# Kernel tuning notes

Hardware: AMD Instinct MI355X
Metric: run time of the kernel (lower is better)

The kernel has to match this reference:

```python
import jax, jax.numpy as jnp
import numpy as np

WEIGHT = 0.1
EPS = 1e-8


def setup_inputs() -> dict:
    key = jax.random.key(0)
    # [B, 3, D, H, W] deformation field
    deformation_field = jax.random.normal(key, (2, 3, 192, 192, 192), dtype=jnp.float32)
    return {"deformation_field": deformation_field}


def reference(deformation_field):
    f = deformation_field
    # jnp.gradient matches torch.gradient defaults: 2nd-order central interior,
    # 1st-order one-sided differences at the edges, unit spacing.
    grad_x = jnp.gradient(f, axis=2)
    grad_y = jnp.gradient(f, axis=3)
    grad_z = jnp.gradient(f, axis=4)

    divergence = grad_x[:, 0:1] + grad_y[:, 1:2] + grad_z[:, 2:3]
    divergence_loss = jnp.mean(divergence ** 2)

    curl_x = grad_z[:, 1:2] - grad_y[:, 2:3]
    curl_y = grad_x[:, 2:3] - grad_z[:, 0:1]
    curl_z = grad_y[:, 0:1] - grad_x[:, 1:2]
    curl_magnitude = jnp.sqrt(curl_x ** 2 + curl_y ** 2 + curl_z ** 2 + EPS)
    curl_loss = jnp.mean(curl_magnitude)

    return WEIGHT * (divergence_loss + curl_loss)
```

## Files before the change

### kernel.cpp

```cpp
#include <hip/hip_runtime.h>


#define DEP 192
#define HGT 192
#define WID 192
#define NB  2

constexpr int SD = HGT * WID;
constexpr int SC = DEP * SD;
constexpr int SB = 3 * SC;
constexpr int W4 = WID / 4;
constexpr int DSEG = 12;
constexpr int NSEG = DEP / DSEG;
constexpr int NG   = NB * NSEG * HGT * W4;
constexpr int NBLK = NG / 256;
constexpr float SCALE = (float)(0.1 / (double)((long long)NB * DEP * HGT * WID));
constexpr float EPS_C = 1e-8f;

struct V4 { float v[4]; };
__device__ __forceinline__ V4 ld4(const float* p) {
    const float4 t = *(const float4*)p;
    V4 r; r.v[0] = t.x; r.v[1] = t.y; r.v[2] = t.z; r.v[3] = t.w; return r;
}

__global__ __launch_bounds__(256, 4) void gcl_kernel(const float* __restrict__ f,
                                                     float* __restrict__ ws) {
    const int g = blockIdx.x * 256 + threadIdx.x;

    int w4 = g % W4;
    int t  = g / W4;
    int h  = t % HGT;
    t /= HGT;
    int ds = t % NSEG;
    int b  = t / NSEG;
    const int w  = w4 * 4;
    const int d0 = ds * DSEG;

    const int   hmi = (h > 0) ? h - 1 : 0;
    const int   hpi = (h < HGT - 1) ? h + 1 : HGT - 1;
    const float sy  = (h == 0 || h == HGT - 1) ? 1.0f : 0.5f;
    const int   dhm = (hmi - h) * WID;
    const int   dhp = (hpi - h) * WID;
    const int   loff = (w > 0) ? -1 : 0;
    const int   roff = (w4 < W4 - 1) ? 4 : 3;
    const float s0w = (w == 0) ? 1.0f : 0.5f;
    const float s3w = (w4 == W4 - 1) ? 1.0f : 0.5f;

    const float* base = f + b * SB + h * WID + w;

    V4 prev[3], cur[3], nxt[3];
    const int pm = (d0 > 0) ? d0 - 1 : 0;
#pragma unroll
    for (int c = 0; c < 3; ++c) {
        const float* pc = base + c * SC;
        prev[c] = ld4(pc + pm * SD);
        cur[c]  = ld4(pc + d0 * SD);
        nxt[c]  = ld4(pc + (d0 + 1) * SD);
    }

    float local = 0.f;

#pragma unroll
    for (int s = 0; s < DSEG; ++s) {
        const int d = d0 + s;

        V4 hm[3], hp[3], nn[3];
        float lv[3], rv[3];
#pragma unroll
        for (int c = 0; c < 3; ++c) {
            const float* pd = base + c * SC + d * SD;
            hm[c] = ld4(pd + dhm);
            hp[c] = ld4(pd + dhp);
            lv[c] = pd[loff];
            rv[c] = pd[roff];
        }
        if (s < DSEG - 1) {
            const int d2 = (d + 2 < DEP) ? d + 2 : DEP - 1;
#pragma unroll
            for (int c = 0; c < 3; ++c)
                nn[c] = ld4(base + c * SC + d2 * SD);
        }

        const float sx = (d == 0 || d == DEP - 1) ? 1.0f : 0.5f;

        float dv[4], cx[4], cy[4], cz[4];
#pragma unroll
        for (int j = 0; j < 4; ++j) {
            dv[j] =  sx * (nxt[0].v[j] - prev[0].v[j]);
            cz[j] = -sx * (nxt[1].v[j] - prev[1].v[j]);
            cy[j] =  sx * (nxt[2].v[j] - prev[2].v[j]);
        }
        {
            float gz0[4], gz1[4], gz2[4];
            gz0[0] = s0w * (cur[0].v[1] - lv[0]);
            gz0[1] = 0.5f * (cur[0].v[2] - cur[0].v[0]);
            gz0[2] = 0.5f * (cur[0].v[3] - cur[0].v[1]);
            gz0[3] = s3w * (rv[0] - cur[0].v[2]);
            gz1[0] = s0w * (cur[1].v[1] - lv[1]);
            gz1[1] = 0.5f * (cur[1].v[2] - cur[1].v[0]);
            gz1[2] = 0.5f * (cur[1].v[3] - cur[1].v[1]);
            gz1[3] = s3w * (rv[1] - cur[1].v[2]);
            gz2[0] = s0w * (cur[2].v[1] - lv[2]);
            gz2[1] = 0.5f * (cur[2].v[2] - cur[2].v[0]);
            gz2[2] = 0.5f * (cur[2].v[3] - cur[2].v[1]);
            gz2[3] = s3w * (rv[2] - cur[2].v[2]);
#pragma unroll
            for (int j = 0; j < 4; ++j) {
                cy[j] -= gz0[j];
                cx[j]  = gz1[j];
                dv[j] += gz2[j];
            }
        }
#pragma unroll
        for (int j = 0; j < 4; ++j) {
            cz[j] += sy * (hp[0].v[j] - hm[0].v[j]);
            dv[j] += sy * (hp[1].v[j] - hm[1].v[j]);
            cx[j] -= sy * (hp[2].v[j] - hm[2].v[j]);
        }
#pragma unroll
        for (int j = 0; j < 4; ++j)
            local += dv[j] * dv[j] +
                     __builtin_amdgcn_sqrtf(cx[j] * cx[j] + cy[j] * cy[j] +
                                            cz[j] * cz[j] + EPS_C);

        if (s < DSEG - 1) {
#pragma unroll
            for (int c = 0; c < 3; ++c) {
                prev[c] = cur[c]; cur[c] = nxt[c]; nxt[c] = nn[c];
            }
        }
    }

#pragma unroll
    for (int off = 32; off > 0; off >>= 1)
        local += __shfl_down(local, off, 64);

    __shared__ float wsum[4];
    const int lane = threadIdx.x & 63;
    const int wv   = threadIdx.x >> 6;
    if (lane == 0) wsum[wv] = local;
    __syncthreads();
    if (threadIdx.x == 0)
        ws[blockIdx.x] = wsum[0] + wsum[1] + wsum[2] + wsum[3];
}

__global__ __launch_bounds__(256) void gcl_reduce(const float* __restrict__ ws,
                                                  float* __restrict__ out) {
    float s = 0.f;
    for (int i = threadIdx.x; i < NBLK; i += 256) s += ws[i];
#pragma unroll
    for (int off = 32; off > 0; off >>= 1)
        s += __shfl_down(s, off, 64);
    __shared__ float wsum[4];
    const int lane = threadIdx.x & 63;
    const int wv   = threadIdx.x >> 6;
    if (lane == 0) wsum[wv] = s;
    __syncthreads();
    if (threadIdx.x == 0)
        out[0] = (wsum[0] + wsum[1] + wsum[2] + wsum[3]) * SCALE;
}

extern "C" void kernel_launch(void* const* d_in, const int* in_sizes, int n_in,
                              void* d_out, int out_size, void* d_ws, size_t ws_size,
                              hipStream_t stream) {
    const float* f = (const float*)d_in[0];
    float* out = (float*)d_out;
    float* ws  = (float*)d_ws;
    gcl_kernel<<<dim3(NBLK), dim3(256), 0, stream>>>(f, ws);
    gcl_reduce<<<dim3(1), dim3(256), 0, stream>>>(ws, out);
}
```

Baseline: 246.5 us.

## Stage 2D tiles in double-buffered LDS for in-plane stencil neighbors

Each block now owns a 16x64 H-W tile and walks 12 depth slices. Each slice is written to double-buffered shared memory along with halo rows and columns. H and W neighbor reads come from LDS instead of redundant global loads. This removes the repeated global and cache traffic for hm/hp/lv/rv, at the cost of one __syncthreads per slice, more LDS use, and divergent halo loads.

New measurement: 577.8 us. +134.4%, slower.

```diff
diff --git a/kernel.cpp b/kernel.cpp
--- a/kernel.cpp
+++ b/kernel.cpp
@@ -9,11 +9,15 @@
 constexpr int SD = HGT * WID;
 constexpr int SC = DEP * SD;
 constexpr int SB = 3 * SC;
-constexpr int W4 = WID / 4;
+constexpr int TH  = 16;
+constexpr int TW4 = 16;
+constexpr int TW  = TW4 * 4;
 constexpr int DSEG = 12;
-constexpr int NSEG = DEP / DSEG;
-constexpr int NG   = NB * NSEG * HGT * W4;
-constexpr int NBLK = NG / 256;
+constexpr int NDS = DEP / DSEG;
+constexpr int NHB = HGT / TH;
+constexpr int NWB = WID / TW;
+constexpr int NBLK = NB * NDS * NHB * NWB;
+constexpr int ROWF = TW + 4;
 constexpr float SCALE = (float)(0.1 / (double)((long long)NB * DEP * HGT * WID));
 constexpr float EPS_C = 1e-8f;
 
@@ -22,100 +26,139 @@
     const float4 t = *(const float4*)p;
     V4 r; r.v[0] = t.x; r.v[1] = t.y; r.v[2] = t.z; r.v[3] = t.w; return r;
 }
+__device__ __forceinline__ void st4(float* p, const V4& a) {
+    *(float4*)p = make_float4(a.v[0], a.v[1], a.v[2], a.v[3]);
+}
 
 __global__ __launch_bounds__(256, 4) void gcl_kernel(const float* __restrict__ f,
                                                      float* __restrict__ ws) {
-    const int g = blockIdx.x * 256 + threadIdx.x;
-
-    int w4 = g % W4;
-    int t  = g / W4;
-    int h  = t % HGT;
-    t /= HGT;
-    int ds = t % NSEG;
-    int b  = t / NSEG;
-    const int w  = w4 * 4;
-    const int d0 = ds * DSEG;
-
-    const int   hmi = (h > 0) ? h - 1 : 0;
-    const int   hpi = (h < HGT - 1) ? h + 1 : HGT - 1;
+    __shared__ float buf[2][3][TH + 2][ROWF];
+    __shared__ float wcol[2][3][TH][2];
+
+    const int tid = threadIdx.x;
+    const int tx = tid & 15;
+    const int ty = tid >> 4;
+
+    int bid = blockIdx.x;
+    const int wb = bid % NWB; bid /= NWB;
+    const int hb = bid % NHB; bid /= NHB;
+    const int dsg = bid % NDS;
+    const int b = bid / NDS;
+
+    const int h0 = hb * TH, w0 = wb * TW, d0 = dsg * DSEG;
+    const int h = h0 + ty;
+    const int w = w0 + tx * 4;
+
     const float sy  = (h == 0 || h == HGT - 1) ? 1.0f : 0.5f;
-    const int   dhm = (hmi - h) * WID;
-    const int   dhp = (hpi - h) * WID;
-    const int   loff = (w > 0) ? -1 : 0;
-    const int   roff = (w4 < W4 - 1) ? 4 : 3;
     const float s0w = (w == 0) ? 1.0f : 0.5f;
-    const float s3w = (w4 == W4 - 1) ? 1.0f : 0.5f;
-
-    const float* base = f + b * SB + h * WID + w;
+    const float s3w = (w + 3 == WID - 1) ? 1.0f : 0.5f;
+
+    const float* fb = f + b * SB;
+    const float* basec = fb + h * WID + w;
+
+    const int  hch  = tid >> 5;
+    const bool hTop = ((tid >> 4) & 1) == 0;
+    const int  htx  = tid & 15;
+    const int  hrow = hTop ? (h0 > 0 ? h0 - 1 : 0)
+                           : (h0 + TH < HGT ? h0 + TH : HGT - 1);
+    const int  hldsrow = hTop ? 0 : TH + 1;
+    const int  cq   = tid - 96;
+    const int  cch  = cq >> 5;
+    const bool cLft = ((cq >> 4) & 1) == 0;
+    const int  crow = cq & 15;
+    const int  ccol = cLft ? (w0 > 0 ? w0 - 1 : 0)
+                           : (w0 + TW < WID ? w0 + TW : WID - 1);
 
     V4 prev[3], cur[3], nxt[3];
     const int pm = (d0 > 0) ? d0 - 1 : 0;
 #pragma unroll
     for (int c = 0; c < 3; ++c) {
-        const float* pc = base + c * SC;
-        prev[c] = ld4(pc + pm * SD);
-        cur[c]  = ld4(pc + d0 * SD);
-        nxt[c]  = ld4(pc + (d0 + 1) * SD);
+        prev[c] = ld4(basec + c * SC + pm * SD);
+        cur[c]  = ld4(basec + c * SC + d0 * SD);
+        nxt[c]  = ld4(basec + c * SC + (d0 + 1) * SD);
     }
+#pragma unroll
+    for (int c = 0; c < 3; ++c)
+        st4(&buf[0][c][ty + 1][tx * 4], cur[c]);
+    if (tid < 96) {
+        const V4 hv = ld4(fb + hch * SC + d0 * SD + hrow * WID + w0 + htx * 4);
+        st4(&buf[0][hch][hldsrow][htx * 4], hv);
+    } else if (tid < 192) {
+        wcol[0][cch][crow][cLft ? 0 : 1] =
+            fb[cch * SC + d0 * SD + (h0 + crow) * WID + ccol];
+    }
+    __syncthreads();
 
     float local = 0.f;
 
 #pragma unroll
     for (int s = 0; s < DSEG; ++s) {
         const int d = d0 + s;
-
-        V4 hm[3], hp[3], nn[3];
-        float lv[3], rv[3];
-#pragma unroll
-        for (int c = 0; c < 3; ++c) {
-            const float* pd = base + c * SC + d * SD;
-            hm[c] = ld4(pd + dhm);
-            hp[c] = ld4(pd + dhp);
-            lv[c] = pd[loff];
-            rv[c] = pd[roff];
-        }
+        const int pb = s & 1, qb = pb ^ 1;
+
+        V4 nn[3];
+        V4 hv = {};
+        float cv = 0.f;
         if (s < DSEG - 1) {
             const int d2 = (d + 2 < DEP) ? d + 2 : DEP - 1;
 #pragma unroll
             for (int c = 0; c < 3; ++c)
-                nn[c] = ld4(base + c * SC + d2 * SD);
+                nn[c] = ld4(basec + c * SC + d2 * SD);
+            if (tid < 96)
+                hv = ld4(fb + hch * SC + (d + 1) * SD + hrow * WID + w0 + htx * 4);
+            else if (tid < 192)
+                cv = fb[cch * SC + (d + 1) * SD + (h0 + crow) * WID + ccol];
+#pragma unroll
+            for (int c = 0; c < 3; ++c)
+                st4(&buf[qb][c][ty + 1][tx * 4], nxt[c]);
         }
 
         const float sx = (d == 0 || d == DEP - 1) ? 1.0f : 0.5f;
-
         float dv[4], cx[4], cy[4], cz[4];
-#pragma unroll
-        for (int j = 0; j < 4; ++j) {
-            dv[j] =  sx * (nxt[0].v[j] - prev[0].v[j]);
-            cz[j] = -sx * (nxt[1].v[j] - prev[1].v[j]);
-            cy[j] =  sx * (nxt[2].v[j] - prev[2].v[j]);
-        }
         {
-            float gz0[4], gz1[4], gz2[4];
-            gz0[0] = s0w * (cur[0].v[1] - lv[0]);
-            gz0[1] = 0.5f * (cur[0].v[2] - cur[0].v[0]);
-            gz0[2] = 0.5f * (cur[0].v[3] - cur[0].v[1]);
-            gz0[3] = s3w * (rv[0] - cur[0].v[2]);
-            gz1[0] = s0w * (cur[1].v[1] - lv[1]);
-            gz1[1] = 0.5f * (cur[1].v[2] - cur[1].v[0]);
-            gz1[2] = 0.5f * (cur[1].v[3] - cur[1].v[1]);
-            gz1[3] = s3w * (rv[1] - cur[1].v[2]);
-            gz2[0] = s0w * (cur[2].v[1] - lv[2]);
-            gz2[1] = 0.5f * (cur[2].v[2] - cur[2].v[0]);
-            gz2[2] = 0.5f * (cur[2].v[3] - cur[2].v[1]);
-            gz2[3] = s3w * (rv[2] - cur[2].v[2]);
+            const V4 hm = ld4(&buf[pb][0][ty][tx * 4]);
+            const V4 hp = ld4(&buf[pb][0][ty + 2][tx * 4]);
+            const float lv = (tx == 0)  ? wcol[pb][0][ty][0] : buf[pb][0][ty + 1][tx * 4 - 1];
+            const float rv = (tx == 15) ? wcol[pb][0][ty][1] : buf[pb][0][ty + 1][tx * 4 + 4];
 #pragma unroll
             for (int j = 0; j < 4; ++j) {
-                cy[j] -= gz0[j];
-                cx[j]  = gz1[j];
-                dv[j] += gz2[j];
-            }
-        }
-#pragma unroll
-        for (int j = 0; j < 4; ++j) {
-            cz[j] += sy * (hp[0].v[j] - hm[0].v[j]);
-            dv[j] += sy * (hp[1].v[j] - hm[1].v[j]);
-            cx[j] -= sy * (hp[2].v[j] - hm[2].v[j]);
+                dv[j] = sx * (nxt[0].v[j] - prev[0].v[j]);
+                cz[j] = sy * (hp.v[j] - hm.v[j]);
+            }
+            cy[0] = -(s0w * (cur[0].v[1] - lv));
+            cy[1] = -(0.5f * (cur[0].v[2] - cur[0].v[0]));
+            cy[2] = -(0.5f * (cur[0].v[3] - cur[0].v[1]));
+            cy[3] = -(s3w * (rv - cur[0].v[2]));
+        }
+        {
+            const V4 hm = ld4(&buf[pb][1][ty][tx * 4]);
+            const V4 hp = ld4(&buf[pb][1][ty + 2][tx * 4]);
+            const float lv = (tx == 0)  ? wcol[pb][1][ty][0] : buf[pb][1][ty + 1][tx * 4 - 1];
+            const float rv = (tx == 15) ? wcol[pb][1][ty][1] : buf[pb][1][ty + 1][tx * 4 + 4];
+#pragma unroll
+            for (int j = 0; j < 4; ++j) {
+                dv[j] += sy * (hp.v[j] - hm.v[j]);
+                cz[j] -= sx * (nxt[1].v[j] - prev[1].v[j]);
+            }
+            cx[0] = s0w * (cur[1].v[1] - lv);
+            cx[1] = 0.5f * (cur[1].v[2] - cur[1].v[0]);
+            cx[2] = 0.5f * (cur[1].v[3] - cur[1].v[1]);
+            cx[3] = s3w * (rv - cur[1].v[2]);
+        }
+        {
+            const V4 hm = ld4(&buf[pb][2][ty][tx * 4]);
+            const V4 hp = ld4(&buf[pb][2][ty + 2][tx * 4]);
+            const float lv = (tx == 0)  ? wcol[pb][2][ty][0] : buf[pb][2][ty + 1][tx * 4 - 1];
+            const float rv = (tx == 15) ? wcol[pb][2][ty][1] : buf[pb][2][ty + 1][tx * 4 + 4];
+            dv[0] += s0w * (cur[2].v[1] - lv);
+            dv[1] += 0.5f * (cur[2].v[2] - cur[2].v[0]);
+            dv[2] += 0.5f * (cur[2].v[3] - cur[2].v[1]);
+            dv[3] += s3w * (rv - cur[2].v[2]);
+#pragma unroll
+            for (int j = 0; j < 4; ++j) {
+                cx[j] -= sy * (hp.v[j] - hm.v[j]);
+                cy[j] += sx * (nxt[2].v[j] - prev[2].v[j]);
+            }
         }
 #pragma unroll
         for (int j = 0; j < 4; ++j)
@@ -124,6 +167,11 @@
                                             cz[j] * cz[j] + EPS_C);
 
         if (s < DSEG - 1) {
+            if (tid < 96)
+                st4(&buf[qb][hch][hldsrow][htx * 4], hv);
+            else if (tid < 192)
+                wcol[qb][cch][crow][cLft ? 0 : 1] = cv;
+            __syncthreads();
 #pragma unroll
             for (int c = 0; c < 3; ++c) {
                 prev[c] = cur[c]; cur[c] = nxt[c]; nxt[c] = nn[c];
@@ -136,11 +184,11 @@
         local += __shfl_down(local, off, 64);
 
     __shared__ float wsum[4];
-    const int lane = threadIdx.x & 63;
-    const int wv   = threadIdx.x >> 6;
+    const int lane = tid & 63;
+    const int wv   = tid >> 6;
     if (lane == 0) wsum[wv] = local;
     __syncthreads();
-    if (threadIdx.x == 0)
+    if (tid == 0)
         ws[blockIdx.x] = wsum[0] + wsum[1] + wsum[2] + wsum[3];
 }
 
```
